# Optimization experiments

Measured on AMD Instinct MI355X. Metric: run time of the kernel, lower is better.

Reference implementation:

```python
import jax, jax.numpy as jnp
import numpy as np

D = 64        # feature dim (== units, required by residual add)
B = 131072    # batch (collocation points)
P = D * (D - 1) // 2  # number of strictly-upper-triangular pairs = 2016

# Static pair indices (i < j), matching row-major boolean_mask of r[:,None] < r
_I, _J = np.triu_indices(D, k=1)
IDX_I = jnp.asarray(_I)
IDX_J = jnp.asarray(_J)


def setup_inputs() -> dict:
    key = jax.random.key(0)
    k1, k2 = jax.random.split(key)
    x = jax.random.normal(k1, (B, D), dtype=jnp.float32)
    # w_init = tf.random_normal_initializer() defaults to stddev=0.05
    w1 = jax.random.normal(k2, (P, D), dtype=jnp.float32) * 0.05
    return {"x": x, "w1": w1}


def reference(x, w1):
    # Pairwise products x_i * x_j for i < j only (avoids full [B, D*D] tensor).
    prod = x[:, IDX_I] * x[:, IDX_J]          # [B, P]
    return jnp.matmul(prod, w1) + x           # [B, D]
```

## Files before the change

kernel.cpp:

```cpp
#include <hip/hip_runtime.h>
#include <hip/hip_bf16.h>
#include <stdint.h>

typedef __attribute__((ext_vector_type(8))) _Float16 half8_t;
typedef __attribute__((ext_vector_type(4))) _Float16 half4_t;
typedef __attribute__((ext_vector_type(2))) _Float16 half2_t;
typedef __attribute__((ext_vector_type(16))) float f32x16;

#define DIM 64
#define NKH 156
#define NSTEP 78
#define BM 256
#define XS_STRIDE 68

struct SchedT { int i[NKH]; int j0[NKH]; };
constexpr SchedT make_sched() {
    SchedT s{};
    int n = 0;
    for (int i = 0; i < 64; ++i)
        for (int jb = (i + 1) >> 4; jb < 4; ++jb) { s.i[n] = i; s.j0[n] = jb * 16; ++n; }
    return s;
}
constexpr SchedT SC = make_sched();

__device__ inline void kg_to_ij(int kg, int& io, int& jo) {
    int cum = 0; io = 0; jo = 0;
    for (int ii = 0; ii < 64; ++ii) {
        int jb0 = (ii + 1) >> 4;
        int nb = 4 - jb0;
        if (kg >= cum && kg < cum + nb) { io = ii; jo = (jb0 + (kg - cum)) * 16; }
        cum += nb;
    }
}

__global__ void wpack_kernel(const float* __restrict__ w1,
                             _Float16* __restrict__ w_h) {
    int id = blockIdx.x * 256 + threadIdx.x;
    if (id >= NSTEP * 4 * 64 * 8) return;
    int e    = id & 7;
    int lane = (id >> 3) & 63;
    int c    = id >> 9;
    int s    = c >> 2;
    int t    = (c >> 1) & 1;
    int h    = c & 1;
    int kg   = s * 2 + h;
    int i, j0;
    kg_to_ij(kg, i, j0);
    int j = j0 + ((lane >> 5) << 3) + e;
    int n = t * 32 + (lane & 31);
    float w = 0.0f;
    if (j > i) {
        int p = i * DIM - (i * (i + 1)) / 2 + (j - i - 1);
        w = w1[p * DIM + n];
    }
    w_h[id] = (_Float16)w;
}

template<int KG, int MT>
__device__ __forceinline__ half8_t aprod(const uint32_t (&xr)[2][32], bool hi) {
    constexpr int I  = SC.i[KG];
    constexpr int J0 = SC.j0[KG];
    constexpr int DI = I >> 1;
    constexpr int DJ = J0 >> 1;
    uint32_t dwi = hi ? xr[MT][DI ^ 4] : xr[MT][DI];
    half2_t hv = __builtin_bit_cast(half2_t, dwi);
    _Float16 xi = hv[I & 1];
    half2_t xi2 = {xi, xi};
    half8_t r;
    half2_t* rp = reinterpret_cast<half2_t*>(&r);
    #pragma unroll
    for (int e2 = 0; e2 < 4; ++e2) {
        half2_t xj = __builtin_bit_cast(half2_t, xr[MT][DJ + e2]);
        rp[e2] = xi2 * xj;
    }
    return r;
}

template<int S>
struct Step {
    static __device__ __forceinline__ void run(const uint32_t (&xr)[2][32],
                                               half8_t (&b)[3][4],
                                               f32x16 (&acc)[2][2],
                                               const half8_t* wl, bool hi) {
        constexpr int SP = (S + 2 < NSTEP) ? S + 2 : NSTEP - 1;
        #pragma unroll
        for (int t = 0; t < 4; ++t)
            b[(S + 2) % 3][t] = wl[(SP * 4 + t) * 64];

        half8_t ah0[2], ah1[2];
        ah0[0] = aprod<S * 2 + 0, 0>(xr, hi);
        ah0[1] = aprod<S * 2 + 0, 1>(xr, hi);
        ah1[0] = aprod<S * 2 + 1, 0>(xr, hi);
        ah1[1] = aprod<S * 2 + 1, 1>(xr, hi);

        #pragma unroll
        for (int mt = 0; mt < 2; ++mt)
            #pragma unroll
            for (int nt = 0; nt < 2; ++nt)
                acc[mt][nt] = __builtin_amdgcn_mfma_f32_32x32x16_f16(
                    ah0[mt], b[S % 3][nt * 2 + 0], acc[mt][nt], 0, 0, 0);
        #pragma unroll
        for (int mt = 0; mt < 2; ++mt)
            #pragma unroll
            for (int nt = 0; nt < 2; ++nt)
                acc[mt][nt] = __builtin_amdgcn_mfma_f32_32x32x16_f16(
                    ah1[mt], b[S % 3][nt * 2 + 1], acc[mt][nt], 0, 0, 0);

        Step<S + 1>::run(xr, b, acc, wl, hi);
    }
};
template<>
struct Step<NSTEP> {
    static __device__ __forceinline__ void run(const uint32_t (&)[2][32], half8_t (&)[3][4],
                                               f32x16 (&)[2][2], const half8_t*, bool) {}
};

__global__ __launch_bounds__(256, 2)
void prodres_kernel(const float* __restrict__ x,
                    const _Float16* __restrict__ w_h,
                    float* __restrict__ out) {
    __shared__ _Float16 xs[BM * XS_STRIDE];

    const int t    = threadIdx.x;
    const int lane = t & 63;
    const int wave = t >> 6;
    const bool hi  = (lane >> 5) & 1;
    const long brow = (long)blockIdx.x * BM;

    #pragma unroll
    for (int it = 0; it < 16; ++it) {
        int row = it * 16 + (t >> 4);
        int c   = (t & 15) * 4;
        float4 v = *reinterpret_cast<const float4*>(x + (brow + row) * DIM + c);
        half4_t hq;
        hq[0] = (_Float16)v.x; hq[1] = (_Float16)v.y;
        hq[2] = (_Float16)v.z; hq[3] = (_Float16)v.w;
        *reinterpret_cast<half4_t*>(&xs[row * XS_STRIDE + c]) = hq;
    }
    __syncthreads();

    uint32_t xr[2][32];
    #pragma unroll
    for (int mt = 0; mt < 2; ++mt) {
        int row = wave * 64 + mt * 32 + (lane & 31);
        const uint32_t* rp = reinterpret_cast<const uint32_t*>(&xs[row * XS_STRIDE]);
        #pragma unroll
        for (int c2 = 0; c2 < 16; ++c2) {
            int src = (2 * c2) ^ (hi ? 4 : 0);
            uint64_t v = *reinterpret_cast<const uint64_t*>(rp + src);
            xr[mt][2 * c2]     = (uint32_t)v;
            xr[mt][2 * c2 + 1] = (uint32_t)(v >> 32);
        }
    }

    f32x16 acc[2][2];
    #pragma unroll
    for (int mt = 0; mt < 2; ++mt)
        #pragma unroll
        for (int nt = 0; nt < 2; ++nt)
            #pragma unroll
            for (int q = 0; q < 16; ++q) acc[mt][nt][q] = 0.0f;

    const half8_t* wl = reinterpret_cast<const half8_t*>(w_h) + lane;
    half8_t b[3][4];

    #pragma unroll
    for (int tt = 0; tt < 4; ++tt) b[0][tt] = wl[tt * 64];
    #pragma unroll
    for (int tt = 0; tt < 4; ++tt) b[1][tt] = wl[(4 + tt) * 64];

    Step<0>::run(xr, b, acc, wl, hi);

    const int hib = hi ? 4 : 0;
    #pragma unroll
    for (int mt = 0; mt < 2; ++mt)
        #pragma unroll
        for (int q = 0; q < 16; ++q) {
            int rit = (q & 3) + 8 * (q >> 2) + hib;
            long row = brow + wave * 64 + mt * 32 + rit;
            #pragma unroll
            for (int nt = 0; nt < 2; ++nt) {
                int col = nt * 32 + (lane & 31);
                out[row * DIM + col] = acc[mt][nt][q] + x[row * DIM + col];
            }
        }
}

extern "C" void kernel_launch(void* const* d_in, const int* in_sizes, int n_in,
                              void* d_out, int out_size, void* d_ws, size_t ws_size,
                              hipStream_t stream) {
    const float* x  = (const float*)d_in[0];
    const float* w1 = (const float*)d_in[1];
    float* out = (float*)d_out;

    _Float16* w_h = (_Float16*)d_ws;

    int b_total = in_sizes[0] / DIM;

    wpack_kernel<<<(NSTEP * 4 * 64 * 8 + 255) / 256, 256, 0, stream>>>(w1, w_h);
    prodres_kernel<<<b_total / BM, 256, 0, stream>>>(x, w_h, out);
}
```

Baseline: 126.2 us.

## Stage packed weights into double-buffered LDS via direct global-to-LDS loads

Each wave no longer fetches its weight fragments from global memory on its own. The 78 K-steps are now grouped into 13 phases of 6 steps. In each phase the block cooperatively loads the next phase's weights straight into an LDS ping-pong buffer with global_load_lds, then syncs at the end of the phase. This shares each weight fetch across the four waves, cutting redundant L2/global traffic and register-held prefetch buffers. The weight buffers reuse the LDS space of the x staging area. Occupancy is raised to 3 blocks per CU. The cost is a block barrier per phase and more register pressure, and correctness depends on the asynchronous LDS loads having completed before the barrier.

```diff
diff --git a/kernel.cpp b/kernel.cpp
--- a/kernel.cpp
+++ b/kernel.cpp
@@ -10,8 +10,13 @@
 #define DIM 64
 #define NKH 156
 #define NSTEP 78
+#define CH 6
+#define NPH 13
 #define BM 256
 #define XS_STRIDE 68
+#define WBUF_HALF (CH * 4 * 512)
+
+static_assert(NPH * CH == NSTEP, "phase tiling");
 
 struct SchedT { int i[NKH]; int j0[NKH]; };
 constexpr SchedT make_sched() {
@@ -76,50 +81,84 @@
     return r;
 }
 
-template<int S>
-struct Step {
+__device__ __forceinline__ void stage_phase(const _Float16* src_lane,
+                                            _Float16* dst_wave,
+                                            int p, int cur) {
+    #pragma unroll
+    for (int k = 0; k < CH; ++k)
+        __builtin_amdgcn_global_load_lds(
+            (const __attribute__((address_space(1))) uint32_t*)(src_lane + (size_t)(p * CH + k) * 2048),
+            (__attribute__((address_space(3))) uint32_t*)(dst_wave + cur * WBUF_HALF + k * 2048),
+            16, 0, 0);
+}
+
+template<int P, int ST>
+struct StepT {
     static __device__ __forceinline__ void run(const uint32_t (&xr)[2][32],
-                                               half8_t (&b)[3][4],
                                                f32x16 (&acc)[2][2],
-                                               const half8_t* wl, bool hi) {
-        constexpr int SP = (S + 2 < NSTEP) ? S + 2 : NSTEP - 1;
-        #pragma unroll
-        for (int t = 0; t < 4; ++t)
-            b[(S + 2) % 3][t] = wl[(SP * 4 + t) * 64];
-
+                                               const _Float16* wbc, int lane, bool hi) {
+        half8_t bb[4];
+        #pragma unroll
+        for (int c = 0; c < 4; ++c)
+            bb[c] = *reinterpret_cast<const half8_t*>(wbc + (ST * 4 + c) * 512 + lane * 8);
+
+        constexpr int KG0 = (P * CH + ST) * 2;
         half8_t ah0[2], ah1[2];
-        ah0[0] = aprod<S * 2 + 0, 0>(xr, hi);
-        ah0[1] = aprod<S * 2 + 0, 1>(xr, hi);
-        ah1[0] = aprod<S * 2 + 1, 0>(xr, hi);
-        ah1[1] = aprod<S * 2 + 1, 1>(xr, hi);
+        ah0[0] = aprod<KG0, 0>(xr, hi);
+        ah0[1] = aprod<KG0, 1>(xr, hi);
+        ah1[0] = aprod<KG0 + 1, 0>(xr, hi);
+        ah1[1] = aprod<KG0 + 1, 1>(xr, hi);
 
         #pragma unroll
         for (int mt = 0; mt < 2; ++mt)
             #pragma unroll
             for (int nt = 0; nt < 2; ++nt)
                 acc[mt][nt] = __builtin_amdgcn_mfma_f32_32x32x16_f16(
-                    ah0[mt], b[S % 3][nt * 2 + 0], acc[mt][nt], 0, 0, 0);
+                    ah0[mt], bb[nt * 2 + 0], acc[mt][nt], 0, 0, 0);
         #pragma unroll
         for (int mt = 0; mt < 2; ++mt)
             #pragma unroll
             for (int nt = 0; nt < 2; ++nt)
                 acc[mt][nt] = __builtin_amdgcn_mfma_f32_32x32x16_f16(
-                    ah1[mt], b[S % 3][nt * 2 + 1], acc[mt][nt], 0, 0, 0);
-
-        Step<S + 1>::run(xr, b, acc, wl, hi);
+                    ah1[mt], bb[nt * 2 + 1], acc[mt][nt], 0, 0, 0);
+
+        StepT<P, ST + 1>::run(xr, acc, wbc, lane, hi);
+    }
+};
+template<int P>
+struct StepT<P, CH> {
+    static __device__ __forceinline__ void run(const uint32_t (&)[2][32], f32x16 (&)[2][2],
+                                               const _Float16*, int, bool) {}
+};
+
+template<int P>
+struct Phase {
+    static __device__ __forceinline__ void run(const uint32_t (&xr)[2][32],
+                                               f32x16 (&acc)[2][2],
+                                               const _Float16* src_lane, _Float16* dst_wave,
+                                               const _Float16* wb, int lane, bool hi) {
+        constexpr int cur = P & 1;
+        if constexpr (P + 1 < NPH)
+            stage_phase(src_lane, const_cast<_Float16*>(dst_wave) - 0, P + 1, cur ^ 1);
+        StepT<P, 0>::run(xr, acc, wb + cur * WBUF_HALF, lane, hi);
+        __syncthreads();
+        Phase<P + 1>::run(xr, acc, src_lane, dst_wave, wb, lane, hi);
     }
 };
 template<>
-struct Step<NSTEP> {
-    static __device__ __forceinline__ void run(const uint32_t (&)[2][32], half8_t (&)[3][4],
-                                               f32x16 (&)[2][2], const half8_t*, bool) {}
-};
-
-__global__ __launch_bounds__(256, 2)
+struct Phase<NPH> {
+    static __device__ __forceinline__ void run(const uint32_t (&)[2][32], f32x16 (&)[2][2],
+                                               const _Float16*, _Float16*, const _Float16*,
+                                               int, bool) {}
+};
+
+__global__ __launch_bounds__(256, 3)
 void prodres_kernel(const float* __restrict__ x,
                     const _Float16* __restrict__ w_h,
                     float* __restrict__ out) {
-    __shared__ _Float16 xs[BM * XS_STRIDE];
+    __shared__ __attribute__((aligned(16))) char smem_raw[2 * WBUF_HALF * 2];
+    _Float16* xs = reinterpret_cast<_Float16*>(smem_raw);
+    _Float16* wb = reinterpret_cast<_Float16*>(smem_raw);
 
     const int t    = threadIdx.x;
     const int lane = t & 63;
@@ -152,6 +191,7 @@
             xr[mt][2 * c2 + 1] = (uint32_t)(v >> 32);
         }
     }
+    __syncthreads();
 
     f32x16 acc[2][2];
     #pragma unroll
@@ -161,15 +201,13 @@
             #pragma unroll
             for (int q = 0; q < 16; ++q) acc[mt][nt][q] = 0.0f;
 
-    const half8_t* wl = reinterpret_cast<const half8_t*>(w_h) + lane;
-    half8_t b[3][4];
-
-    #pragma unroll
-    for (int tt = 0; tt < 4; ++tt) b[0][tt] = wl[tt * 64];
-    #pragma unroll
-    for (int tt = 0; tt < 4; ++tt) b[1][tt] = wl[(4 + tt) * 64];
-
-    Step<0>::run(xr, b, acc, wl, hi);
+    const _Float16* src_lane = w_h + wave * 512 + lane * 8;
+    _Float16* dst_wave = wb + wave * 512;
+
+    stage_phase(src_lane, dst_wave, 0, 0);
+    __syncthreads();
+
+    Phase<0>::run(xr, acc, src_lane, dst_wave, wb, lane, hi);
 
     const int hib = hi ? 4 : 0;
     #pragma unroll
```

New measurement: 140.5 us. 1.11x slower.
